# Kernel tuning notes

Measured on AMD Instinct MI355X. Metric: run time of the kernel, lower is better.

Reference implementation:

```python
import jax, jax.numpy as jnp
import numpy as np

PATCH = 3  # patch_size, padding = PATCH//2 = 1, stride = 1
EPS = 1e-12  # F.normalize eps


def extract_patches(x):
    """F.unfold(k=3, stride=1, pad=1) then reshape to [B, N, C, 3, 3] (N=H*W)."""
    b, c, h, w = x.shape
    xp = jnp.pad(x, ((0, 0), (0, 0), (1, 1), (1, 1)))
    # stack the 9 shifted views: [B, C, 9, H, W]; order (kh, kw) matches torch unfold
    shifts = [xp[:, :, i:i + h, j:j + w] for i in range(PATCH) for j in range(PATCH)]
    p = jnp.stack(shifts, axis=2)
    p = p.reshape(b, c, PATCH, PATCH, h * w)
    return jnp.transpose(p, (0, 4, 1, 2, 3))  # [B, N, C, 3, 3]


def cosine_similarity(x, y):
    """x, y: [B, N, ...] patch sets -> [B, Nx, Ny] cosine similarity."""
    b = x.shape[0]
    xf = x.reshape(b, x.shape[1], -1)
    yf = y.reshape(b, y.shape[1], -1)
    xn = xf / jnp.maximum(jnp.linalg.norm(xf, axis=2, keepdims=True), EPS)
    yn = yf / jnp.maximum(jnp.linalg.norm(yf, axis=2, keepdims=True), EPS)
    return jnp.einsum('bnd,bmd->bnm', xn, yn)


def setup_inputs() -> dict:
    key = jax.random.key(0)
    k1, k2, k3, k4 = jax.random.split(key, 4)
    B, C, H, W = 2, 64, 80, 80
    return {
        'content_feat': jax.random.normal(k1, (B, C, H, W), dtype=jnp.float32),
        'style_feat': jax.random.normal(k2, (B, C, H, W), dtype=jnp.float32),
        'content_mask': jax.random.uniform(k3, (B, 3, H, W), dtype=jnp.float32),
        'style_mask': jax.random.uniform(k4, (B, 3, H, W), dtype=jnp.float32),
    }


def reference(content_feat, style_feat, content_mask, style_mask):
    content_patches = extract_patches(content_feat)      # [B, N, C, 3, 3]
    style_patches = extract_patches(style_feat)          # [B, N, C, 3, 3]
    cmask_patches = extract_patches(content_mask)        # [B, N, 3, 3, 3]
    smask_patches = extract_patches(style_mask)          # [B, N, 3, 3, 3]

    feat_sim = cosine_similarity(content_patches, style_patches)   # [B, N, N]
    mask_sim = cosine_similarity(cmask_patches, smask_patches)     # [B, N, N]
    similarity = feat_sim * mask_sim

    best = jnp.argmax(similarity, axis=2)                # [B, N]
    b, n = best.shape
    sp_flat = style_patches.reshape(b, n, -1)            # [B, N, C*9]
    matched = jnp.take_along_axis(sp_flat, best[:, :, None], axis=1)
    return matched.reshape(style_patches.shape)          # [B, N, C, 3, 3]
```

## Files before the change

### kernel.cpp

```cpp
#include <hip/hip_runtime.h>

#define HH 80
#define WW 80
#define NPIX 6400
#define PW 82
#define NPP (PW*PW)
#define CFE 64
#define CMA 3
#define KF 576
#define GUARD 1024
#define NREG 8

#define PA 1024
#define POUT 856
#define BW 1056

typedef unsigned long long u64;
typedef unsigned int u32;

__device__ __forceinline__ void gload4(const float* g, float* l) {
    __builtin_amdgcn_global_load_lds((const __attribute__((address_space(1))) void*)g,
                                     (__attribute__((address_space(3))) void*)l, 4, 0, 0);
}
__device__ __forceinline__ float4 ld4(const float* p) { return *(const float4*)p; }

__global__ __launch_bounds__(256)
void pixsq_kernel(const float* __restrict__ sf, const float* __restrict__ sm,
                  float* __restrict__ psf, float* __restrict__ psm) {
    int g = blockIdx.x * 256 + threadIdx.x;
    if (g >= 2 * NPIX) return;
    int b = g / NPIX, m = g - b * NPIX;
    const float* p = sf + (size_t)b * CFE * NPIX + m;
    float a = 0.f;
    #pragma unroll 8
    for (int c = 0; c < CFE; ++c) { float v = p[c * NPIX]; a = fmaf(v, v, a); }
    const float* q = sm + (size_t)b * CMA * NPIX + m;
    float am = 0.f;
    #pragma unroll
    for (int c = 0; c < CMA; ++c) { float v = q[c * NPIX]; am = fmaf(v, v, am); }
    psf[g] = a; psm[g] = am;
}

__global__ __launch_bounds__(256)
void rn2_kernel(const float* __restrict__ psf, const float* __restrict__ psm,
                float* __restrict__ rn2) {
    int g = blockIdx.x * 256 + threadIdx.x;
    if (g >= 2 * NPIX) return;
    int b = g / NPIX, m = g - b * NPIX;
    int mh = m / WW, mw = m - mh * WW;
    float sF = 0.f, sM = 0.f;
    #pragma unroll
    for (int di = -1; di <= 1; ++di) {
        if ((unsigned)(mh + di) >= HH) continue;
        #pragma unroll
        for (int dj = -1; dj <= 1; ++dj) {
            if ((unsigned)(mw + dj) >= WW) continue;
            int mm = m + di * WW + dj;
            sF += psf[b * NPIX + mm];
            sM += psm[b * NPIX + mm];
        }
    }
    float rf = 1.f / fmaxf(sqrtf(sF), 1e-12f);
    float rm = 1.f / fmaxf(sqrtf(sM), 1e-12f);
    rn2[g] = rf * rm;
}

__global__ __launch_bounds__(256)
void pad_kernel(const float* __restrict__ cf, const float* __restrict__ sf,
                const float* __restrict__ cm, const float* __restrict__ sm,
                float* __restrict__ cfp, float* __restrict__ sfp,
                float* __restrict__ cmp, float* __restrict__ smp) {
    int gid = blockIdx.x * 256 + threadIdx.x;
    if (gid >= 2 * 2 * 67 * NPIX) return;
    int pix = gid % NPIX; int t = gid / NPIX;
    int c = t % 67; t /= 67;
    int b = t & 1; int which = t >> 1;
    int h = pix / WW, w = pix - h * WW;
    int qq = (h + 1) * PW + (w + 1);
    if (which == 0) {
        if (c < 64) cfp[((size_t)b * CFE + c) * NPP + qq] = cf[((size_t)b * CFE + c) * NPIX + pix];
        else        cmp[((size_t)b * CMA + (c - 64)) * NPP + qq] = cm[((size_t)b * CMA + (c - 64)) * NPIX + pix];
    } else {
        if (c < 64) sfp[((size_t)b * CFE + c) * NPP + qq] = sf[((size_t)b * CFE + c) * NPIX + pix];
        else        smp[((size_t)b * CMA + (c - 64)) * NPP + qq] = sm[((size_t)b * CMA + (c - 64)) * NPIX + pix];
    }
}

__global__ __launch_bounds__(1024, 4)
void fuse_kernel(const float* __restrict__ cfp, const float* __restrict__ sfp,
                 const float* __restrict__ cmp, const float* __restrict__ smp,
                 const float* __restrict__ rn2, u64* __restrict__ pbest) {
    const int dt = blockIdx.x;
    const int pt = blockIdx.y;
    const int b  = blockIdx.z;
    const int pstart = 83 + POUT * pt;
    const int pend   = min(pstart + POUT, 6641);
    const int pbase  = pstart - 84;
    const int d0     = -6560 + 32 * dt;
    if (pend - 1 + d0 + 31 < 83 || pstart + d0 > 6640) return;

    __shared__ float pool[PA * 36];

    const int tid = threadIdx.x;
    const int tp = tid & 255;
    const int tg = tid >> 8;
    const int wb = tid & 960;

    const float* cfb = cfp + (size_t)b * CFE * NPP + pbase;
    const float* sfb = sfp + (size_t)b * CFE * NPP + pbase + d0;
    const float* cmb = cmp + (size_t)b * CMA * NPP + pbase;
    const float* smb = smp + (size_t)b * CMA * NPP + pbase + d0;

    float acc[4][8];
    float pdF[32], pdM[32];

    auto zacc = [&]() {
        #pragma unroll
        for (int k = 0; k < 4; ++k)
            #pragma unroll
            for (int j = 0; j < 8; ++j) acc[k][j] = 0.f;
    };

    auto stageF = [&](int q, int buf) {
        float* Ab = pool + buf * 16640;
        float* Bb = Ab + 8 * PA;
        const float* As = cfb + (size_t)(q * 8) * NPP;
        const float* Bs = sfb + (size_t)(q * 8) * NPP;
        #pragma unroll
        for (int cc = 0; cc < 8; ++cc) {
            gload4(As + cc * NPP + tid, Ab + cc * PA + wb);
            gload4(Bs + cc * NPP + tid, Bb + cc * BW + wb);
            if (tid < 32) gload4(Bs + cc * NPP + 1024 + tid, Bb + cc * BW + 1024);
        }
    };

    auto gemmc = [&](const float* Ab, const float* Bb) {
        const float* Ar = Ab + 4 * tp;
        const float* Br = Bb + 4 * tp + 8 * tg;
        float a[4], bb[12];
        *(float4*)a        = ld4(Ar);
        *(float4*)bb       = ld4(Br);
        *(float4*)(bb + 4) = ld4(Br + 4);
        *(float4*)(bb + 8) = ld4(Br + 8);
        #pragma unroll
        for (int k = 0; k < 4; ++k)
            #pragma unroll
            for (int j = 0; j < 8; ++j)
                acc[k][j] = fmaf(a[k], bb[k + j], acc[k][j]);
    };

    auto s0write = [&]() {
        #pragma unroll
        for (int k = 0; k < 4; ++k) {
            float* d = pool + (4 * tp + k) * 36 + 8 * tg;
            *(float4*)d       = make_float4(acc[k][0], acc[k][1], acc[k][2], acc[k][3]);
            *(float4*)(d + 4) = make_float4(acc[k][4], acc[k][5], acc[k][6], acc[k][7]);
        }
    };

    auto tapsrun = [&](float (&pd)[32]) {
        const int row = tid;
        if (row < 84 || row >= 84 + POUT) return;
        const float* Lr = pool + row * 36;
        #pragma unroll
        for (int j4 = 0; j4 < 8; ++j4) {
            float4 v = ld4(Lr - 83 * 36 + 4 * j4);
            float4 t;
            t = ld4(Lr - 82 * 36 + 4 * j4); v.x += t.x; v.y += t.y; v.z += t.z; v.w += t.w;
            t = ld4(Lr - 81 * 36 + 4 * j4); v.x += t.x; v.y += t.y; v.z += t.z; v.w += t.w;
            t = ld4(Lr -      36 + 4 * j4); v.x += t.x; v.y += t.y; v.z += t.z; v.w += t.w;
            t = ld4(Lr           + 4 * j4); v.x += t.x; v.y += t.y; v.z += t.z; v.w += t.w;
            t = ld4(Lr +      36 + 4 * j4); v.x += t.x; v.y += t.y; v.z += t.z; v.w += t.w;
            t = ld4(Lr + 81 * 36 + 4 * j4); v.x += t.x; v.y += t.y; v.z += t.z; v.w += t.w;
            t = ld4(Lr + 82 * 36 + 4 * j4); v.x += t.x; v.y += t.y; v.z += t.z; v.w += t.w;
            t = ld4(Lr + 83 * 36 + 4 * j4); v.x += t.x; v.y += t.y; v.z += t.z; v.w += t.w;
            pd[j4 * 4 + 0] = v.x; pd[j4 * 4 + 1] = v.y;
            pd[j4 * 4 + 2] = v.z; pd[j4 * 4 + 3] = v.w;
        }
    };

    zacc();
    stageF(0, 0);
    __syncthreads();
    int buf = 0;
    #pragma unroll 1
    for (int q = 0; q < 8; ++q) {
        if (q < 7) stageF(q + 1, buf ^ 1);
        const float* Ab = pool + buf * 16640;
        const float* Bb = Ab + 8 * PA;
        #pragma unroll 2
        for (int cc = 0; cc < 8; ++cc)
            gemmc(Ab + cc * PA, Bb + cc * BW);
        __syncthreads();
        buf ^= 1;
    }
    s0write();
    __syncthreads();
    tapsrun(pdF);
    __syncthreads();

    #pragma unroll
    for (int cc = 0; cc < 3; ++cc) {
        gload4(cmb + cc * NPP + tid, pool + cc * PA + wb);
        gload4(smb + cc * NPP + tid, pool + 3 * PA + cc * BW + wb);
        if (tid < 32) gload4(smb + cc * NPP + 1024 + tid, pool + 3 * PA + cc * BW + 1024);
    }
    __syncthreads();
    zacc();
    #pragma unroll
    for (int cc = 0; cc < 3; ++cc)
        gemmc(pool + cc * PA, pool + 3 * PA + cc * BW);
    __syncthreads();
    s0write();
    __syncthreads();
    tapsrun(pdM);

    const float* rb = rn2 + b * NPIX;
    u64* pb = pbest + ((size_t)(dt & (NREG - 1)) * 2 + b) * NPIX;
    {
        const int row = tid;
        const int p = pbase + row;
        if (row >= 84 && p < pend) {
            int ph = p / PW, pw2 = p - ph * PW;
            if (ph >= 1 && ph <= 80 && pw2 >= 1 && pw2 <= 80) {
                int n_real = (ph - 1) * 80 + (pw2 - 1);
                u64 key = 0;
                #pragma unroll
                for (int j = 0; j < 32; ++j) {
                    int m = p + d0 + j;
                    if (m < 83 || m > 6640) continue;
                    int mh = m / PW, mw = m - mh * PW;
                    if (mw < 1 || mw > 80) continue;
                    int mr = (mh - 1) * 80 + (mw - 1);
                    float sc = pdF[j] * pdM[j] * rb[mr];
                    sc += 0.f;
                    u32 u = __float_as_uint(sc);
                    u ^= (u >> 31) ? 0xFFFFFFFFu : 0x80000000u;
                    u64 k2 = ((u64)u << 32) | (u32)~(u32)mr;
                    if (k2 > key) key = k2;
                }
                if (key) {
                    u64 cur = pb[n_real];
                    if (key > cur) atomicMax(&pb[n_real], key);
                }
            }
        }
    }
}

__global__ __launch_bounds__(64)
void gather_kernel(const float* __restrict__ sf, const u64* __restrict__ pbest,
                   float* __restrict__ out) {
    int n = blockIdx.x, b = blockIdx.y;
    int lane = threadIdx.x;

    u64 key = 0;
    #pragma unroll
    for (int r = 0; r < NREG; ++r) {
        u64 k = pbest[((size_t)r * 2 + b) * NPIX + n];
        if (k > key) key = k;
    }
    int m = (int)(~(u32)key);
    if ((unsigned)m >= NPIX) m = 0;
    int mh = m / WW, mw = m - mh * WW;
    const float* sfb = sf + (size_t)b * CFE * NPIX;
    float* ob = out + ((size_t)b * NPIX + n) * (size_t)KF;
    #pragma unroll
    for (int e = lane; e < KF; e += 64) {
        int c = e / 9, pos = e - c * 9;
        int di = pos / 3 - 1, dj = pos - (pos / 3) * 3 - 1;
        int h = mh + di, w = mw + dj;
        ob[e] = ((unsigned)h < HH && (unsigned)w < WW) ? sfb[c * NPIX + h * WW + w] : 0.f;
    }
}

extern "C" void kernel_launch(void* const* d_in, const int* in_sizes, int n_in,
                              void* d_out, int out_size, void* d_ws, size_t ws_size,
                              hipStream_t stream) {
    const float* cf = (const float*)d_in[0];
    const float* sf = (const float*)d_in[1];
    const float* cm = (const float*)d_in[2];
    const float* sm = (const float*)d_in[3];
    float* out = (float*)d_out;

    float* psf = (float*)d_ws;
    float* psm = psf + 2 * NPIX;
    float* rn2 = psm + 2 * NPIX;
    u64*  pbest = (u64*)(rn2 + 2 * NPIX);
    float* padreg = (float*)(pbest + (size_t)NREG * 2 * NPIX);
    float* cfp = padreg + GUARD;
    float* sfp = cfp + (size_t)2 * CFE * NPP + GUARD;
    float* cmp = sfp + (size_t)2 * CFE * NPP + GUARD;
    float* smp = cmp + (size_t)2 * CMA * NPP + GUARD;

    size_t zero_bytes = (size_t)NREG * 2 * NPIX * 8 +
        ((size_t)5 * GUARD + 2 * ((size_t)2 * CFE * NPP) + 2 * ((size_t)2 * CMA * NPP)) * 4;
    hipMemsetAsync(pbest, 0, zero_bytes, stream);

    pad_kernel<<<(2 * 2 * 67 * NPIX + 255) / 256, 256, 0, stream>>>(
        cf, sf, cm, sm, cfp, sfp, cmp, smp);
    pixsq_kernel<<<(2 * NPIX + 255) / 256, 256, 0, stream>>>(sf, sm, psf, psm);
    rn2_kernel  <<<(2 * NPIX + 255) / 256, 256, 0, stream>>>(psf, psm, rn2);

    fuse_kernel<<<dim3(410, 8, 2), 1024, 0, stream>>>(cfp, sfp, cmp, smp, rn2, pbest);

    gather_kernel<<<dim3(NPIX, 2), 64, 0, stream>>>(sf, pbest, out);
}
```

Measured before the change: 620.3 us.

## Halve fuse block size, double per-thread diagonal tile, trim empty blocks, swizzle LDS

The fuse kernel drops from 1024 to 512 threads per block, and each thread now accumulates 16 diagonals instead of 8, so A-fragment reuse per thread doubles. The grid x range is computed per row-tile so only diagonal tiles that overlap valid outputs are launched, removing many early-exit blocks. The LDS layout for the correlation results is XOR-swizzled to cut bank conflicts in the 9-tap sum. The normalisation table is stored in padded coordinates, where a zero value marks the border, which replaces the per-candidate div/mod index math. In exchange, per-thread register pressure rises (64 accumulators plus two 32-entry partial arrays).

```diff
diff --git a/kernel.cpp b/kernel.cpp
--- a/kernel.cpp
+++ b/kernel.cpp
@@ -43,7 +43,7 @@
 
 __global__ __launch_bounds__(256)
 void rn2_kernel(const float* __restrict__ psf, const float* __restrict__ psm,
-                float* __restrict__ rn2) {
+                float* __restrict__ rn2p) {
     int g = blockIdx.x * 256 + threadIdx.x;
     if (g >= 2 * NPIX) return;
     int b = g / NPIX, m = g - b * NPIX;
@@ -62,7 +62,7 @@
     }
     float rf = 1.f / fmaxf(sqrtf(sF), 1e-12f);
     float rm = 1.f / fmaxf(sqrtf(sM), 1e-12f);
-    rn2[g] = rf * rm;
+    rn2p[(size_t)b * NPP + (mh + 1) * PW + (mw + 1)] = rf * rm;
 }
 
 __global__ __launch_bounds__(256)
@@ -86,39 +86,42 @@
     }
 }
 
-__global__ __launch_bounds__(1024, 4)
+__global__ __launch_bounds__(512, 2)
 void fuse_kernel(const float* __restrict__ cfp, const float* __restrict__ sfp,
                  const float* __restrict__ cmp, const float* __restrict__ smp,
-                 const float* __restrict__ rn2, u64* __restrict__ pbest) {
-    const int dt = blockIdx.x;
+                 const float* __restrict__ rn2p, u64* __restrict__ pbest) {
     const int pt = blockIdx.y;
     const int b  = blockIdx.z;
     const int pstart = 83 + POUT * pt;
     const int pend   = min(pstart + POUT, 6641);
     const int pbase  = pstart - 84;
-    const int d0     = -6560 + 32 * dt;
-    if (pend - 1 + d0 + 31 < 83 || pstart + d0 > 6640) return;
+    const int dte0   = (6644 - pend) >> 5;
+    const int dtemax = (13200 - pstart) >> 5;
+    const int dte = dte0 + blockIdx.x;
+    if (dte > dtemax) return;
+    const int d0 = -6560 + 32 * dte;
 
     __shared__ float pool[PA * 36];
 
     const int tid = threadIdx.x;
     const int tp = tid & 255;
     const int tg = tid >> 8;
-    const int wb = tid & 960;
+    const int wb = tid & 448;
+    const int swz = (tp & 7) << 2;
 
     const float* cfb = cfp + (size_t)b * CFE * NPP + pbase;
     const float* sfb = sfp + (size_t)b * CFE * NPP + pbase + d0;
     const float* cmb = cmp + (size_t)b * CMA * NPP + pbase;
     const float* smb = smp + (size_t)b * CMA * NPP + pbase + d0;
 
-    float acc[4][8];
-    float pdF[32], pdM[32];
+    float acc[4][16];
+    float pdF[2][32], pdM[2][32];
 
     auto zacc = [&]() {
         #pragma unroll
         for (int k = 0; k < 4; ++k)
             #pragma unroll
-            for (int j = 0; j < 8; ++j) acc[k][j] = 0.f;
+            for (int j = 0; j < 16; ++j) acc[k][j] = 0.f;
     };
 
     auto stageF = [&](int q, int buf) {
@@ -128,54 +131,63 @@
         const float* Bs = sfb + (size_t)(q * 8) * NPP;
         #pragma unroll
         for (int cc = 0; cc < 8; ++cc) {
-            gload4(As + cc * NPP + tid, Ab + cc * PA + wb);
-            gload4(Bs + cc * NPP + tid, Bb + cc * BW + wb);
+            gload4(As + cc * NPP + tid,       Ab + cc * PA + wb);
+            gload4(As + cc * NPP + 512 + tid, Ab + cc * PA + 512 + wb);
+            gload4(Bs + cc * NPP + tid,       Bb + cc * BW + wb);
+            gload4(Bs + cc * NPP + 512 + tid, Bb + cc * BW + 512 + wb);
             if (tid < 32) gload4(Bs + cc * NPP + 1024 + tid, Bb + cc * BW + 1024);
         }
     };
 
     auto gemmc = [&](const float* Ab, const float* Bb) {
         const float* Ar = Ab + 4 * tp;
-        const float* Br = Bb + 4 * tp + 8 * tg;
-        float a[4], bb[12];
-        *(float4*)a        = ld4(Ar);
-        *(float4*)bb       = ld4(Br);
-        *(float4*)(bb + 4) = ld4(Br + 4);
-        *(float4*)(bb + 8) = ld4(Br + 8);
+        const float* Br = Bb + 4 * tp + 16 * tg;
+        float a[4], bb[20];
+        *(float4*)a         = ld4(Ar);
+        *(float4*)bb        = ld4(Br);
+        *(float4*)(bb + 4)  = ld4(Br + 4);
+        *(float4*)(bb + 8)  = ld4(Br + 8);
+        *(float4*)(bb + 12) = ld4(Br + 12);
+        *(float4*)(bb + 16) = ld4(Br + 16);
         #pragma unroll
         for (int k = 0; k < 4; ++k)
             #pragma unroll
-            for (int j = 0; j < 8; ++j)
+            for (int j = 0; j < 16; ++j)
                 acc[k][j] = fmaf(a[k], bb[k + j], acc[k][j]);
     };
 
     auto s0write = [&]() {
         #pragma unroll
         for (int k = 0; k < 4; ++k) {
-            float* d = pool + (4 * tp + k) * 36 + 8 * tg;
-            *(float4*)d       = make_float4(acc[k][0], acc[k][1], acc[k][2], acc[k][3]);
-            *(float4*)(d + 4) = make_float4(acc[k][4], acc[k][5], acc[k][6], acc[k][7]);
-        }
-    };
-
-    auto tapsrun = [&](float (&pd)[32]) {
-        const int row = tid;
-        if (row < 84 || row >= 84 + POUT) return;
-        const float* Lr = pool + row * 36;
-        #pragma unroll
-        for (int j4 = 0; j4 < 8; ++j4) {
-            float4 v = ld4(Lr - 83 * 36 + 4 * j4);
-            float4 t;
-            t = ld4(Lr - 82 * 36 + 4 * j4); v.x += t.x; v.y += t.y; v.z += t.z; v.w += t.w;
-            t = ld4(Lr - 81 * 36 + 4 * j4); v.x += t.x; v.y += t.y; v.z += t.z; v.w += t.w;
-            t = ld4(Lr -      36 + 4 * j4); v.x += t.x; v.y += t.y; v.z += t.z; v.w += t.w;
-            t = ld4(Lr           + 4 * j4); v.x += t.x; v.y += t.y; v.z += t.z; v.w += t.w;
-            t = ld4(Lr +      36 + 4 * j4); v.x += t.x; v.y += t.y; v.z += t.z; v.w += t.w;
-            t = ld4(Lr + 81 * 36 + 4 * j4); v.x += t.x; v.y += t.y; v.z += t.z; v.w += t.w;
-            t = ld4(Lr + 82 * 36 + 4 * j4); v.x += t.x; v.y += t.y; v.z += t.z; v.w += t.w;
-            t = ld4(Lr + 83 * 36 + 4 * j4); v.x += t.x; v.y += t.y; v.z += t.z; v.w += t.w;
-            pd[j4 * 4 + 0] = v.x; pd[j4 * 4 + 1] = v.y;
-            pd[j4 * 4 + 2] = v.z; pd[j4 * 4 + 3] = v.w;
+            float* dr = pool + (4 * tp + k) * 36;
+            #pragma unroll
+            for (int g = 0; g < 4; ++g) {
+                *(float4*)(dr + ((16 * tg + 4 * g) ^ swz)) =
+                    make_float4(acc[k][4 * g], acc[k][4 * g + 1],
+                                acc[k][4 * g + 2], acc[k][4 * g + 3]);
+            }
+        }
+    };
+
+    auto tapsrun = [&](float (&pd)[2][32]) {
+        #pragma unroll
+        for (int s = 0; s < 2; ++s) {
+            const int row = tid + 512 * s;
+            if (row < 84 || row >= 84 + POUT) continue;
+            #pragma unroll
+            for (int j4 = 0; j4 < 8; ++j4) {
+                float4 v = make_float4(0.f, 0.f, 0.f, 0.f);
+                #pragma unroll
+                for (int t9 = 0; t9 < 9; ++t9) {
+                    static const int dlt[9] = {-83, -82, -81, -1, 0, 1, 81, 82, 83};
+                    const int rr = row + dlt[t9];
+                    const int sw = ((rr >> 2) & 7) << 2;
+                    float4 t = ld4(pool + rr * 36 + ((4 * j4) ^ sw));
+                    v.x += t.x; v.y += t.y; v.z += t.z; v.w += t.w;
+                }
+                pd[s][4 * j4 + 0] = v.x; pd[s][4 * j4 + 1] = v.y;
+                pd[s][4 * j4 + 2] = v.z; pd[s][4 * j4 + 3] = v.w;
+            }
         }
     };
 
@@ -201,8 +213,10 @@
 
     #pragma unroll
     for (int cc = 0; cc < 3; ++cc) {
-        gload4(cmb + cc * NPP + tid, pool + cc * PA + wb);
-        gload4(smb + cc * NPP + tid, pool + 3 * PA + cc * BW + wb);
+        gload4(cmb + cc * NPP + tid,       pool + cc * PA + wb);
+        gload4(cmb + cc * NPP + 512 + tid, pool + cc * PA + 512 + wb);
+        gload4(smb + cc * NPP + tid,       pool + 3 * PA + cc * BW + wb);
+        gload4(smb + cc * NPP + 512 + tid, pool + 3 * PA + cc * BW + 512 + wb);
         if (tid < 32) gload4(smb + cc * NPP + 1024 + tid, pool + 3 * PA + cc * BW + 1024);
     }
     __syncthreads();
@@ -215,35 +229,33 @@
     __syncthreads();
     tapsrun(pdM);
 
-    const float* rb = rn2 + b * NPIX;
-    u64* pb = pbest + ((size_t)(dt & (NREG - 1)) * 2 + b) * NPIX;
-    {
-        const int row = tid;
+    const float* rb = rn2p + (size_t)b * NPP;
+    u64* pb = pbest + ((size_t)(dte & (NREG - 1)) * 2 + b) * NPIX;
+    #pragma unroll
+    for (int s = 0; s < 2; ++s) {
+        const int row = tid + 512 * s;
         const int p = pbase + row;
-        if (row >= 84 && p < pend) {
-            int ph = p / PW, pw2 = p - ph * PW;
-            if (ph >= 1 && ph <= 80 && pw2 >= 1 && pw2 <= 80) {
-                int n_real = (ph - 1) * 80 + (pw2 - 1);
-                u64 key = 0;
-                #pragma unroll
-                for (int j = 0; j < 32; ++j) {
-                    int m = p + d0 + j;
-                    if (m < 83 || m > 6640) continue;
-                    int mh = m / PW, mw = m - mh * PW;
-                    if (mw < 1 || mw > 80) continue;
-                    int mr = (mh - 1) * 80 + (mw - 1);
-                    float sc = pdF[j] * pdM[j] * rb[mr];
-                    sc += 0.f;
-                    u32 u = __float_as_uint(sc);
-                    u ^= (u >> 31) ? 0xFFFFFFFFu : 0x80000000u;
-                    u64 k2 = ((u64)u << 32) | (u32)~(u32)mr;
-                    if (k2 > key) key = k2;
-                }
-                if (key) {
-                    u64 cur = pb[n_real];
-                    if (key > cur) atomicMax(&pb[n_real], key);
-                }
-            }
+        if (row < 84 || p >= pend) continue;
+        int ph = p / PW, pw2 = p - ph * PW;
+        if (ph < 1 || ph > 80 || pw2 < 1 || pw2 > 80) continue;
+        int n_real = (ph - 1) * 80 + (pw2 - 1);
+        u64 key = 0;
+        #pragma unroll
+        for (int j = 0; j < 32; ++j) {
+            int mp = p + d0 + j;
+            if ((unsigned)mp >= (unsigned)NPP) continue;
+            float r2 = rb[mp];
+            if (r2 == 0.f) continue;
+            float sc = pdF[s][j] * pdM[s][j] * r2;
+            sc += 0.f;
+            u32 u = __float_as_uint(sc);
+            u ^= (u >> 31) ? 0xFFFFFFFFu : 0x80000000u;
+            u64 k2 = ((u64)u << 32) | (u32)~(u32)mp;
+            if (k2 > key) key = k2;
+        }
+        if (key) {
+            u64 cur = pb[n_real];
+            if (key > cur) atomicMax(&pb[n_real], key);
         }
     }
 }
@@ -260,8 +272,13 @@
         u64 k = pbest[((size_t)r * 2 + b) * NPIX + n];
         if (k > key) key = k;
     }
-    int m = (int)(~(u32)key);
-    if ((unsigned)m >= NPIX) m = 0;
+    int mp = (int)(~(u32)key);
+    int m = 0;
+    if ((unsigned)mp < (unsigned)NPP) {
+        int ph = mp / PW, pw = mp - ph * PW;
+        if (ph >= 1 && ph <= 80 && pw >= 1 && pw <= 80)
+            m = (ph - 1) * 80 + (pw - 1);
+    }
     int mh = m / WW, mw = m - mh * WW;
     const float* sfb = sf + (size_t)b * CFE * NPIX;
     float* ob = out + ((size_t)b * NPIX + n) * (size_t)KF;
@@ -285,24 +302,25 @@
 
     float* psf = (float*)d_ws;
     float* psm = psf + 2 * NPIX;
-    float* rn2 = psm + 2 * NPIX;
-    u64*  pbest = (u64*)(rn2 + 2 * NPIX);
-    float* padreg = (float*)(pbest + (size_t)NREG * 2 * NPIX);
+    u64*  pbest = (u64*)(psm + 2 * NPIX);
+    float* rn2p = (float*)(pbest + (size_t)NREG * 2 * NPIX);
+    float* padreg = rn2p + 2 * NPP;
     float* cfp = padreg + GUARD;
     float* sfp = cfp + (size_t)2 * CFE * NPP + GUARD;
     float* cmp = sfp + (size_t)2 * CFE * NPP + GUARD;
     float* smp = cmp + (size_t)2 * CMA * NPP + GUARD;
 
     size_t zero_bytes = (size_t)NREG * 2 * NPIX * 8 +
-        ((size_t)5 * GUARD + 2 * ((size_t)2 * CFE * NPP) + 2 * ((size_t)2 * CMA * NPP)) * 4;
+        ((size_t)2 * NPP + (size_t)5 * GUARD +
+         (size_t)4 * CFE * NPP + (size_t)4 * CMA * NPP) * 4;
     hipMemsetAsync(pbest, 0, zero_bytes, stream);
 
     pad_kernel<<<(2 * 2 * 67 * NPIX + 255) / 256, 256, 0, stream>>>(
         cf, sf, cm, sm, cfp, sfp, cmp, smp);
     pixsq_kernel<<<(2 * NPIX + 255) / 256, 256, 0, stream>>>(sf, sm, psf, psm);
-    rn2_kernel  <<<(2 * NPIX + 255) / 256, 256, 0, stream>>>(psf, psm, rn2);
-
-    fuse_kernel<<<dim3(410, 8, 2), 1024, 0, stream>>>(cfp, sfp, cmp, smp, rn2, pbest);
+    rn2_kernel  <<<(2 * NPIX + 255) / 256, 256, 0, stream>>>(psf, psm, rn2p);
+
+    fuse_kernel<<<dim3(232, 8, 2), 512, 0, stream>>>(cfp, sfp, cmp, smp, rn2p, pbest);
 
     gather_kernel<<<dim3(NPIX, 2), 64, 0, stream>>>(sf, pbest, out);
 }
```

New measurement: 684.4 us. +10.3%, slower.
